# Kernel tuning notes

Measured on AMD Instinct MI355X. Metric: run time of the kernel, lower is better.

Reference implementation:

```python
import jax, jax.numpy as jnp
import numpy as np

GROUP_IDX = np.array([[(0, 1, 2), (3, 0, 1), (2, 3, 0), (1, 2, 3)][g % 4] for g in range(20)])
PAULI_Z = np.array([1.0, -1.0], dtype=np.float32)
RAND_WIRES = [3, 1, 0, 2]  # frozen structure standing in for qml.RandomLayers(seed=42)


def apply_1q(state, U, w):
    # state: (2,2,2,2) complex, U: (2,2)
    s = jnp.tensordot(U, state, axes=([1], [w]))
    return jnp.moveaxis(s, 0, w)


def apply_cnot(state, c, t):
    s = jnp.moveaxis(state, (c, t), (0, 1))
    s = s.at[1].set(s[1, ::-1])  # flip target where control == 1
    return jnp.moveaxis(s, (0, 1), (c, t))


def rot_mat(phi, theta, omega):
    # qml.Rot = RZ(phi) -> RY(theta) -> RZ(omega)
    c, s = jnp.cos(theta / 2), jnp.sin(theta / 2)
    ep = jnp.exp(-0.5j * (phi + omega))
    em = jnp.exp(0.5j * (phi - omega))
    return jnp.stack([jnp.stack([ep * c, -em * s]), jnp.stack([jnp.conj(em) * s, jnp.conj(ep) * c])])


def rx_mat(t):
    c, s = jnp.cos(t / 2), jnp.sin(t / 2)
    return jnp.stack([jnp.stack([c + 0j, -1j * s]), jnp.stack([-1j * s, c + 0j])])


def ry_mat(t):
    c, s = jnp.cos(t / 2), jnp.sin(t / 2)
    return jnp.stack([jnp.stack([c + 0j, -s + 0j]), jnp.stack([s + 0j, c + 0j])])


def rz_mat(t):
    e0, e1 = jnp.exp(-0.5j * t), jnp.exp(0.5j * t)
    z = jnp.zeros_like(e0)
    return jnp.stack([jnp.stack([e0, z]), jnp.stack([z, e1])])


def circuit(patch, rand_params):
    # patch: (4,) pixels of one 2x2 block
    angles = patch[GROUP_IDX] * np.pi  # (20, 3): (phi, theta, omega) per group
    state = jnp.zeros((2, 2, 2, 2), jnp.complex64).at[0, 0, 0, 0].set(1.0)

    def step(state, abc):
        U = rot_mat(abc[0], abc[1], abc[2])
        for j in range(4):
            state = apply_1q(state, U, j)
            for k in range(3):
                state = apply_cnot(state, k, k + 1)
            state = apply_cnot(state, 3, 0)
        return state, None

    state, _ = jax.lax.scan(step, state, angles)
    # deterministic stand-in for RandomLayers(rand_params)
    p = rand_params.reshape(-1)
    mats = [rx_mat, ry_mat, rz_mat, rx_mat]
    for i in range(4):
        state = apply_1q(state, mats[i](p[i]), RAND_WIRES[i])
        if i == 1:
            state = apply_cnot(state, 0, 2)
        if i == 3:
            state = apply_cnot(state, 1, 3)
    probs = jnp.real(state * jnp.conj(state))  # (2,2,2,2)
    z = jnp.asarray(PAULI_Z)
    ev = [jnp.sum(probs * z.reshape([2 if a == j else 1 for a in range(4)])) for j in range(4)]
    return jnp.stack(ev)  # (4,) PauliZ expvals


def setup_inputs() -> dict:
    key = jax.random.key(0)
    k1, k2, k3, k4 = jax.random.split(key, 4)
    images = jax.random.uniform(k1, (64, 1, 28, 28), dtype=jnp.float32)
    rand_params = jax.random.uniform(k2, (1, 4), dtype=jnp.float32, maxval=2.0 * np.pi)
    fc_w = jax.random.normal(k3, (10, 784), dtype=jnp.float32) * 0.05
    fc_b = jax.random.normal(k4, (10,), dtype=jnp.float32) * 0.05
    return {"images": images, "rand_params": rand_params, "fc_w": fc_w, "fc_b": fc_b}


def reference(images, rand_params, fc_w, fc_b):
    b = images.shape[0]
    # 2x2 non-overlapping patches, order [p(j,k), p(j,k+1), p(j+1,k), p(j+1,k+1)]
    patches = images[:, 0].reshape(b, 14, 2, 14, 2).transpose(0, 1, 3, 2, 4).reshape(b, 196, 4)
    q = jax.vmap(jax.vmap(circuit, in_axes=(0, None)), in_axes=(0, None))(patches, rand_params)
    logits = q.reshape(b, -1) @ fc_w.T + fc_b  # (b, 10)
    return jax.nn.log_softmax(logits, axis=1)
```

## Files before the change

kernel.cpp:

```cpp
#include <hip/hip_runtime.h>
#include <math.h>

#define PI_F 3.14159265358979323846f


struct Gates { int xm[84]; int sm[84]; int fin[4]; };

constexpr Gates make_gates() {
  Gates gt{};
  int F[4] = {1, 2, 4, 8};
  int H[4] = {1, 2, 4, 8};
  int ng = 0;
  auto cnot = [&](int c, int t) {
    const int pc = 3 - c, pt = 3 - t;
    F[pt] ^= F[pc];
    for (int p = 0; p < 4; ++p)
      if (H[p] & (1 << pt)) H[p] ^= (1 << pc);
  };
  auto gate = [&](int w) {
    const int p = 3 - w;
    int m = 0;
    for (int q = 0; q < 4; ++q)
      if (H[q] & (1 << p)) m |= 1 << q;
    gt.xm[ng] = m; gt.sm[ng] = F[p]; ++ng;
  };
  for (int step = 0; step < 20; ++step)
    for (int j = 0; j < 4; ++j) {
      gate(j);
      cnot(0, 1); cnot(1, 2); cnot(2, 3); cnot(3, 0);
    }
  gate(3); gate(1); cnot(0, 2); gate(0); gate(2); cnot(1, 3);
  for (int p = 0; p < 4; ++p) gt.fin[p] = F[p];
  return gt;
}

constexpr Gates GT = make_gates();

#define APPLY_GATE(K, WR, WI, XR, XI) do {                                    \
    const float pre_ = __shfl_xor(re, GT.xm[K]);                              \
    const float pim_ = __shfl_xor(im, GT.xm[K]);                              \
    const unsigned sb_ = (unsigned)(__popc(l16 & GT.sm[K]) & 1) << 31;        \
    const float cmi_ = __uint_as_float(__float_as_uint(WI) ^ sb_);            \
    const float cpr_ = __uint_as_float(__float_as_uint(XR) ^ sb_);            \
    const float nre_ = (WR)*re - cmi_*im + cpr_*pre_ - (XI)*pim_;             \
    const float nim_ = (WR)*im + cmi_*re + cpr_*pim_ + (XI)*pre_;             \
    re = nre_; im = nim_;                                                     \
  } while (0)

__global__ __launch_bounds__(256) void qcnn_circuit_kernel(
    const float* __restrict__ images,
    const float* __restrict__ rp,
    float* __restrict__ qout)
{
  const int gtid = blockIdx.x * 256 + threadIdx.x;
  const int c    = gtid >> 4;
  const int l16  = gtid & 15;

  const int b  = c / 196;
  const int pi = c - b * 196;
  const int pj = pi / 14;
  const int pk = pi - pj * 14;

  const float* img = images + b * 784 + (2 * pj) * 28 + 2 * pk;
  float px[4];
  px[0] = img[0]  * PI_F;
  px[1] = img[1]  * PI_F;
  px[2] = img[28] * PI_F;
  px[3] = img[29] * PI_F;

  float wr[4], wi[4], xr[4], xi[4];
  {
    const int GIphi[4] = {0, 3, 2, 1};
    const int GIth [4] = {1, 0, 3, 2};
    const int GIom [4] = {2, 1, 0, 3};
#pragma unroll
    for (int g = 0; g < 4; ++g) {
      const float phi = px[GIphi[g]], th = px[GIth[g]], om = px[GIom[g]];
      const float a = 0.5f * (phi + om), d = 0.5f * (phi - om), h = 0.5f * th;
      const float sa = __sinf(a), ca = __cosf(a);
      const float sd = __sinf(d), cd = __cosf(d);
      const float st = __sinf(h), ct = __cosf(h);
      wr[g] =  ca * ct;  wi[g] = -sa * ct;
      xr[g] = -cd * st;  xi[g] = -sd * st;
    }
  }

  float re = (l16 == 0) ? 1.f : 0.f;
  float im = 0.f;

#pragma unroll
  for (int step = 0; step < 20; ++step) {
    const int g = step & 3;
#pragma unroll
    for (int j = 0; j < 4; ++j) {
      const int k = step * 4 + j;
      APPLY_GATE(k, wr[g], wi[g], xr[g], xi[g]);
    }
  }

  {
    const float s0 = __sinf(0.5f * rp[0]), c0 = __cosf(0.5f * rp[0]);
    APPLY_GATE(80, c0, 0.f, 0.f, -s0);
    const float s1 = __sinf(0.5f * rp[1]), c1 = __cosf(0.5f * rp[1]);
    APPLY_GATE(81, c1, 0.f, -s1, 0.f);
    const float s2 = __sinf(0.5f * rp[2]), c2 = __cosf(0.5f * rp[2]);
    APPLY_GATE(82, c2, -s2, 0.f, 0.f);
    const float s3 = __sinf(0.5f * rp[3]), c3 = __cosf(0.5f * rp[3]);
    APPLY_GATE(83, c3, 0.f, 0.f, -s3);
  }

  const float pr = re * re + im * im;
  float e0 = __uint_as_float(__float_as_uint(pr) ^ ((unsigned)(__popc(l16 & GT.fin[3]) & 1) << 31));
  float e1 = __uint_as_float(__float_as_uint(pr) ^ ((unsigned)(__popc(l16 & GT.fin[2]) & 1) << 31));
  float e2 = __uint_as_float(__float_as_uint(pr) ^ ((unsigned)(__popc(l16 & GT.fin[1]) & 1) << 31));
  float e3 = __uint_as_float(__float_as_uint(pr) ^ ((unsigned)(__popc(l16 & GT.fin[0]) & 1) << 31));
#pragma unroll
  for (int s = 1; s < 16; s <<= 1) {
    e0 += __shfl_xor(e0, s);
    e1 += __shfl_xor(e1, s);
    e2 += __shfl_xor(e2, s);
    e3 += __shfl_xor(e3, s);
  }
  float v = e0;
  v = (l16 == 1) ? e1 : v;
  v = (l16 == 2) ? e2 : v;
  v = (l16 == 3) ? e3 : v;
  if (l16 < 4) qout[c * 4 + l16] = v;
}

__global__ __launch_bounds__(64) void qcnn_fc_kernel(
    const float* __restrict__ q,
    const float* __restrict__ fcw,
    const float* __restrict__ fcb,
    float* __restrict__ out)
{
  const int b    = blockIdx.x;
  const int lane = threadIdx.x;
  const float4* q4 = reinterpret_cast<const float4*>(q + b * 784);
  const float4* w4 = reinterpret_cast<const float4*>(fcw);

  float acc[10];
#pragma unroll
  for (int o = 0; o < 10; ++o) acc[o] = 0.f;

  for (int i = lane; i < 196; i += 64) {
    const float4 qv = q4[i];
#pragma unroll
    for (int o = 0; o < 10; ++o) {
      const float4 wv = w4[o * 196 + i];
      acc[o] += qv.x * wv.x + qv.y * wv.y + qv.z * wv.z + qv.w * wv.w;
    }
  }

#pragma unroll
  for (int o = 0; o < 10; ++o) {
    for (int off = 32; off > 0; off >>= 1)
      acc[o] += __shfl_down(acc[o], off);
  }

  if (lane == 0) {
    float logits[10];
    float mx = -1e30f;
#pragma unroll
    for (int o = 0; o < 10; ++o) {
      logits[o] = acc[o] + fcb[o];
      mx = fmaxf(mx, logits[o]);
    }
    float se = 0.f;
#pragma unroll
    for (int o = 0; o < 10; ++o) se += __expf(logits[o] - mx);
    const float lse = mx + __logf(se);
#pragma unroll
    for (int o = 0; o < 10; ++o) out[b * 10 + o] = logits[o] - lse;
  }
}


extern "C" void kernel_launch(void* const* d_in, const int* in_sizes, int n_in,
                              void* d_out, int out_size, void* d_ws, size_t ws_size,
                              hipStream_t stream) {
  const float* images = (const float*)d_in[0];
  const float* rp     = (const float*)d_in[1];
  const float* fcw    = (const float*)d_in[2];
  const float* fcb    = (const float*)d_in[3];
  float* out = (float*)d_out;
  float* q   = (float*)d_ws;

  qcnn_circuit_kernel<<<784, 256, 0, stream>>>(images, rp, q);
  qcnn_fc_kernel<<<64, 64, 0, stream>>>(q, fcw, fcb, out);
}
```

Before: 19.68 us.

## Fuse circuit and FC/log-softmax into one kernel with last-block reduction

Merges the quantum-circuit kernel and the FC + log-softmax kernel into a single launch. Each block handles 16 patches of one image, multiplies the expectation values by the FC weights in-register, reduces them across the wavefront and block, and writes per-block partial logits. An atomic counter selects the last of the 13 blocks per image to finish the log-softmax. Parity sign bits now come from a precomputed lookup mask instead of popc. The cost is a memset launch, atomics with thread fences, and some padded idle patches in the last block of each image.

```diff
diff --git a/kernel.cpp b/kernel.cpp
--- a/kernel.cpp
+++ b/kernel.cpp
@@ -39,7 +39,7 @@
 #define APPLY_GATE(K, WR, WI, XR, XI) do {                                    \
     const float pre_ = __shfl_xor(re, GT.xm[K]);                              \
     const float pim_ = __shfl_xor(im, GT.xm[K]);                              \
-    const unsigned sb_ = (unsigned)(__popc(l16 & GT.sm[K]) & 1) << 31;        \
+    const unsigned sb_ = ((P >> GT.sm[K]) & 1u) << 31;                        \
     const float cmi_ = __uint_as_float(__float_as_uint(WI) ^ sb_);            \
     const float cpr_ = __uint_as_float(__float_as_uint(XR) ^ sb_);            \
     const float nre_ = (WR)*re - cmi_*im + cpr_*pre_ - (XI)*pim_;             \
@@ -47,131 +47,155 @@
     re = nre_; im = nim_;                                                     \
   } while (0)
 
-__global__ __launch_bounds__(256) void qcnn_circuit_kernel(
+__global__ __launch_bounds__(256) void qcnn_fused_kernel(
     const float* __restrict__ images,
     const float* __restrict__ rp,
-    float* __restrict__ qout)
-{
-  const int gtid = blockIdx.x * 256 + threadIdx.x;
-  const int c    = gtid >> 4;
-  const int l16  = gtid & 15;
-
-  const int b  = c / 196;
-  const int pi = c - b * 196;
-  const int pj = pi / 14;
-  const int pk = pi - pj * 14;
-
-  const float* img = images + b * 784 + (2 * pj) * 28 + 2 * pk;
-  float px[4];
-  px[0] = img[0]  * PI_F;
-  px[1] = img[1]  * PI_F;
-  px[2] = img[28] * PI_F;
-  px[3] = img[29] * PI_F;
-
-  float wr[4], wi[4], xr[4], xi[4];
-  {
-    const int GIphi[4] = {0, 3, 2, 1};
-    const int GIth [4] = {1, 0, 3, 2};
-    const int GIom [4] = {2, 1, 0, 3};
-#pragma unroll
-    for (int g = 0; g < 4; ++g) {
-      const float phi = px[GIphi[g]], th = px[GIth[g]], om = px[GIom[g]];
-      const float a = 0.5f * (phi + om), d = 0.5f * (phi - om), h = 0.5f * th;
-      const float sa = __sinf(a), ca = __cosf(a);
-      const float sd = __sinf(d), cd = __cosf(d);
-      const float st = __sinf(h), ct = __cosf(h);
-      wr[g] =  ca * ct;  wi[g] = -sa * ct;
-      xr[g] = -cd * st;  xi[g] = -sd * st;
-    }
-  }
-
-  float re = (l16 == 0) ? 1.f : 0.f;
-  float im = 0.f;
-
-#pragma unroll
-  for (int step = 0; step < 20; ++step) {
-    const int g = step & 3;
-#pragma unroll
-    for (int j = 0; j < 4; ++j) {
-      const int k = step * 4 + j;
-      APPLY_GATE(k, wr[g], wi[g], xr[g], xi[g]);
-    }
-  }
-
-  {
-    const float s0 = __sinf(0.5f * rp[0]), c0 = __cosf(0.5f * rp[0]);
-    APPLY_GATE(80, c0, 0.f, 0.f, -s0);
-    const float s1 = __sinf(0.5f * rp[1]), c1 = __cosf(0.5f * rp[1]);
-    APPLY_GATE(81, c1, 0.f, -s1, 0.f);
-    const float s2 = __sinf(0.5f * rp[2]), c2 = __cosf(0.5f * rp[2]);
-    APPLY_GATE(82, c2, -s2, 0.f, 0.f);
-    const float s3 = __sinf(0.5f * rp[3]), c3 = __cosf(0.5f * rp[3]);
-    APPLY_GATE(83, c3, 0.f, 0.f, -s3);
-  }
-
-  const float pr = re * re + im * im;
-  float e0 = __uint_as_float(__float_as_uint(pr) ^ ((unsigned)(__popc(l16 & GT.fin[3]) & 1) << 31));
-  float e1 = __uint_as_float(__float_as_uint(pr) ^ ((unsigned)(__popc(l16 & GT.fin[2]) & 1) << 31));
-  float e2 = __uint_as_float(__float_as_uint(pr) ^ ((unsigned)(__popc(l16 & GT.fin[1]) & 1) << 31));
-  float e3 = __uint_as_float(__float_as_uint(pr) ^ ((unsigned)(__popc(l16 & GT.fin[0]) & 1) << 31));
-#pragma unroll
-  for (int s = 1; s < 16; s <<= 1) {
-    e0 += __shfl_xor(e0, s);
-    e1 += __shfl_xor(e1, s);
-    e2 += __shfl_xor(e2, s);
-    e3 += __shfl_xor(e3, s);
-  }
-  float v = e0;
-  v = (l16 == 1) ? e1 : v;
-  v = (l16 == 2) ? e2 : v;
-  v = (l16 == 3) ? e3 : v;
-  if (l16 < 4) qout[c * 4 + l16] = v;
-}
-
-__global__ __launch_bounds__(64) void qcnn_fc_kernel(
-    const float* __restrict__ q,
     const float* __restrict__ fcw,
     const float* __restrict__ fcb,
-    float* __restrict__ out)
+    float* __restrict__ out,
+    int*   __restrict__ cnt,
+    float* __restrict__ partials)
 {
-  const int b    = blockIdx.x;
-  const int lane = threadIdx.x;
-  const float4* q4 = reinterpret_cast<const float4*>(q + b * 784);
-  const float4* w4 = reinterpret_cast<const float4*>(fcw);
+  const int tid = threadIdx.x;
+  const int B   = blockIdx.x;
+  const int b   = B / 13;
+  const int sb  = B - b * 13;
+  const int grp = tid >> 4;
+  const int l16 = tid & 15;
+  const int pi  = sb * 16 + grp;
+  const bool active = (pi < 196);
+
+  unsigned P = 0;
+  if (l16 & 1) P ^= 0xAAAAu;
+  if (l16 & 2) P ^= 0xCCCCu;
+  if (l16 & 4) P ^= 0xF0F0u;
+  if (l16 & 8) P ^= 0xFF00u;
+
+  float val = 0.f;
+
+  if (active) {
+    const int pj = pi / 14;
+    const int pk = pi - pj * 14;
+    const float* img = images + b * 784 + (2 * pj) * 28 + 2 * pk;
+    float px[4];
+    px[0] = img[0]  * PI_F;
+    px[1] = img[1]  * PI_F;
+    px[2] = img[28] * PI_F;
+    px[3] = img[29] * PI_F;
+
+    float wr[4], wi[4], xr[4], xi[4];
+    {
+      const int GIphi[4] = {0, 3, 2, 1};
+      const int GIth [4] = {1, 0, 3, 2};
+      const int GIom [4] = {2, 1, 0, 3};
+#pragma unroll
+      for (int g = 0; g < 4; ++g) {
+        const float phi = px[GIphi[g]], th = px[GIth[g]], om = px[GIom[g]];
+        const float a = 0.5f * (phi + om), d = 0.5f * (phi - om), h = 0.5f * th;
+        const float sa = __sinf(a), ca = __cosf(a);
+        const float sd = __sinf(d), cd = __cosf(d);
+        const float st = __sinf(h), ct = __cosf(h);
+        wr[g] =  ca * ct;  wi[g] = -sa * ct;
+        xr[g] = -cd * st;  xi[g] = -sd * st;
+      }
+    }
+
+    float re = (l16 == 0) ? 1.f : 0.f;
+    float im = 0.f;
+
+#pragma unroll
+    for (int step = 0; step < 20; ++step) {
+      const int g = step & 3;
+#pragma unroll
+      for (int j = 0; j < 4; ++j) {
+        const int k = step * 4 + j;
+        APPLY_GATE(k, wr[g], wi[g], xr[g], xi[g]);
+      }
+    }
+
+    {
+      const float s0 = __sinf(0.5f * rp[0]), c0 = __cosf(0.5f * rp[0]);
+      APPLY_GATE(80, c0, 0.f, 0.f, -s0);
+      const float s1 = __sinf(0.5f * rp[1]), c1 = __cosf(0.5f * rp[1]);
+      APPLY_GATE(81, c1, 0.f, -s1, 0.f);
+      const float s2 = __sinf(0.5f * rp[2]), c2 = __cosf(0.5f * rp[2]);
+      APPLY_GATE(82, c2, -s2, 0.f, 0.f);
+      const float s3 = __sinf(0.5f * rp[3]), c3 = __cosf(0.5f * rp[3]);
+      APPLY_GATE(83, c3, 0.f, 0.f, -s3);
+    }
+
+    const float pr = re * re + im * im;
+    float e0 = __uint_as_float(__float_as_uint(pr) ^ (((P >> GT.fin[3]) & 1u) << 31));
+    float e1 = __uint_as_float(__float_as_uint(pr) ^ (((P >> GT.fin[2]) & 1u) << 31));
+    float e2 = __uint_as_float(__float_as_uint(pr) ^ (((P >> GT.fin[1]) & 1u) << 31));
+    float e3 = __uint_as_float(__float_as_uint(pr) ^ (((P >> GT.fin[0]) & 1u) << 31));
+#pragma unroll
+    for (int s = 1; s < 16; s <<= 1) {
+      e0 += __shfl_xor(e0, s);
+      e1 += __shfl_xor(e1, s);
+      e2 += __shfl_xor(e2, s);
+      e3 += __shfl_xor(e3, s);
+    }
+    val = (l16 == 0) ? e0 : (l16 == 1) ? e1 : (l16 == 2) ? e2 : (l16 == 3) ? e3 : 0.f;
+  }
 
   float acc[10];
-#pragma unroll
-  for (int o = 0; o < 10; ++o) acc[o] = 0.f;
-
-  for (int i = lane; i < 196; i += 64) {
-    const float4 qv = q4[i];
-#pragma unroll
-    for (int o = 0; o < 10; ++o) {
-      const float4 wv = w4[o * 196 + i];
-      acc[o] += qv.x * wv.x + qv.y * wv.y + qv.z * wv.z + qv.w * wv.w;
-    }
-  }
-
+  if (l16 < 4) {
+    const int fidx = pi * 4 + l16;
+#pragma unroll
+    for (int o = 0; o < 10; ++o) acc[o] = val * fcw[o * 784 + fidx];
+  } else {
+#pragma unroll
+    for (int o = 0; o < 10; ++o) acc[o] = 0.f;
+  }
 #pragma unroll
   for (int o = 0; o < 10; ++o) {
-    for (int off = 32; off > 0; off >>= 1)
-      acc[o] += __shfl_down(acc[o], off);
-  }
-
-  if (lane == 0) {
-    float logits[10];
-    float mx = -1e30f;
-#pragma unroll
-    for (int o = 0; o < 10; ++o) {
-      logits[o] = acc[o] + fcb[o];
-      mx = fmaxf(mx, logits[o]);
-    }
-    float se = 0.f;
-#pragma unroll
-    for (int o = 0; o < 10; ++o) se += __expf(logits[o] - mx);
-    const float lse = mx + __logf(se);
-#pragma unroll
-    for (int o = 0; o < 10; ++o) out[b * 10 + o] = logits[o] - lse;
+    acc[o] += __shfl_xor(acc[o], 16);
+    acc[o] += __shfl_xor(acc[o], 32);
+    acc[o] += __shfl_xor(acc[o], 1);
+    acc[o] += __shfl_xor(acc[o], 2);
+  }
+
+  __shared__ float wacc[4][10];
+  __shared__ int lastflag;
+  const int wid = tid >> 6;
+  if ((tid & 63) == 0) {
+#pragma unroll
+    for (int o = 0; o < 10; ++o) wacc[wid][o] = acc[o];
+  }
+  __syncthreads();
+  if (tid < 10) {
+    const float ps = wacc[0][tid] + wacc[1][tid] + wacc[2][tid] + wacc[3][tid];
+    partials[(b * 13 + sb) * 10 + tid] = ps;
+  }
+  __syncthreads();
+
+  if (tid == 0) {
+    __threadfence();
+    const int old = atomicAdd(&cnt[b], 1);
+    lastflag = (old == 12);
+  }
+  __syncthreads();
+
+  if (lastflag) {
+    __threadfence();
+    if (tid < 16) {
+      float lgv = -1e30f;
+      if (tid < 10) {
+        float s = fcb[tid];
+#pragma unroll
+        for (int k = 0; k < 13; ++k) s += partials[(b * 13 + k) * 10 + tid];
+        lgv = s;
+      }
+      float mx = lgv;
+#pragma unroll
+      for (int s = 1; s < 16; s <<= 1) mx = fmaxf(mx, __shfl_xor(mx, s));
+      float ex = (tid < 10) ? __expf(lgv - mx) : 0.f;
+      float se = ex;
+#pragma unroll
+      for (int s = 1; s < 16; s <<= 1) se += __shfl_xor(se, s);
+      if (tid < 10) out[b * 10 + tid] = lgv - mx - __logf(se);
+    }
   }
 }
 
@@ -184,8 +208,10 @@
   const float* fcw    = (const float*)d_in[2];
   const float* fcb    = (const float*)d_in[3];
   float* out = (float*)d_out;
-  float* q   = (float*)d_ws;
-
-  qcnn_circuit_kernel<<<784, 256, 0, stream>>>(images, rp, q);
-  qcnn_fc_kernel<<<64, 64, 0, stream>>>(q, fcw, fcb, out);
+
+  int*   cnt      = (int*)d_ws;
+  float* partials = (float*)d_ws + 64;
+
+  hipMemsetAsync(cnt, 0, 64 * sizeof(int), stream);
+  qcnn_fused_kernel<<<832, 256, 0, stream>>>(images, rp, fcw, fcb, out, cnt, partials);
 }
```

Result: slower. 43.74 us (+122.3%).
